# Optimization experiments

Hardware: AMD Instinct MI355X
Metric: run time of the kernel (lower is better)

## Reference

```python
import jax, jax.numpy as jnp
import numpy as np

N_X = 50000      # real nodes
N_MOTIF = 10000  # motif nodes
N = N_X + N_MOTIF
E = 1_920_000    # edges (avg degree 32)
NFEAT = 512
NHID = 256
PAD_N = 65536


def setup_inputs() -> dict:
    key = jax.random.key(0)
    ks = jax.random.split(key, 12)
    x = jax.random.normal(ks[0], (N_X, NFEAT), dtype=jnp.float32)
    motif_emb = jax.random.normal(ks[1], (N_MOTIF, NFEAT), dtype=jnp.float32)
    adj_rows = jax.random.randint(ks[2], (E,), 0, N)
    adj_cols = jax.random.randint(ks[3], (E,), 0, N)
    adj_vals = jax.random.uniform(ks[4], (E,), dtype=jnp.float32)
    # unique scatter positions (torch output[pos_idx]=x with distinct indices)
    pos_idx = jax.random.permutation(ks[5], PAD_N)[:N_X]
    # GraphConvolution params (pygcn style: support = x@W; out = spmm(adj, support) + b)
    s1 = 1.0 / np.sqrt(NHID)
    w1 = jax.random.uniform(ks[6], (NFEAT, NHID), minval=-s1, maxval=s1, dtype=jnp.float32)
    b1 = jax.random.uniform(ks[7], (NHID,), minval=-s1, maxval=s1, dtype=jnp.float32)
    w2 = jax.random.uniform(ks[8], (NHID, NHID), minval=-s1, maxval=s1, dtype=jnp.float32)
    b2 = jax.random.uniform(ks[9], (NHID,), minval=-s1, maxval=s1, dtype=jnp.float32)
    w3 = jax.random.uniform(ks[10], (NHID, NHID), minval=-s1, maxval=s1, dtype=jnp.float32)
    b3 = jax.random.uniform(ks[11], (NHID,), minval=-s1, maxval=s1, dtype=jnp.float32)
    return {"x": x, "motif_emb": motif_emb, "adj_rows": adj_rows, "adj_cols": adj_cols,
            "adj_vals": adj_vals, "pos_idx": pos_idx, "pad_n": PAD_N,
            "w1": w1, "b1": b1, "w2": w2, "b2": b2, "w3": w3, "b3": b3}


def _gcn_layer(h, rows, cols, vals, w, b):
    support = h @ w                                   # [N, nhid]
    msgs = vals[:, None] * support[cols]              # [E, nhid]
    agg = jax.ops.segment_sum(msgs, rows, num_segments=N)  # spmm(adj, support)
    return jax.nn.relu(agg + b)


def reference(x, motif_emb, adj_rows, adj_cols, adj_vals, pos_idx, pad_n,
              w1, b1, w2, b2, w3, b3):
    h = jnp.concatenate((x, motif_emb), axis=0)       # [N, nfeat]
    h = _gcn_layer(h, adj_rows, adj_cols, adj_vals, w1, b1)
    # dropout is identity in eval mode
    h = _gcn_layer(h, adj_rows, adj_cols, adj_vals, w2, b2)
    h = _gcn_layer(h, adj_rows, adj_cols, adj_vals, w3, b3)
    h = h[:N_X]                                       # drop motif nodes
    output = jnp.zeros((pad_n, h.shape[1]), dtype=h.dtype)
    output = output.at[pos_idx].set(h)                # irregular scatter-assign
    return output
```

## Files before the change

### kernel.cpp

```cpp
#include <hip/hip_runtime.h>

#define N_TOTAL 60000
#define N_X     50000
#define N_EDGE  1920000
#define NFEAT   512
#define NHID    256
#define SLOTS   96
#define NCHUNK  8

typedef __attribute__((ext_vector_type(8))) short bf16x8;
typedef __attribute__((ext_vector_type(4))) float f32x4;
typedef __attribute__((ext_vector_type(4))) unsigned u32x4;

__device__ __forceinline__ unsigned short f2bf(float f) {
    unsigned u = __float_as_uint(f);
    unsigned r = (u + 0x7FFFu + ((u >> 16) & 1u)) >> 16;
    return (unsigned short)r;
}
__device__ __forceinline__ float bf_lo(unsigned u) { return __uint_as_float(u << 16); }
__device__ __forceinline__ float bf_hi(unsigned u) { return __uint_as_float(u & 0xFFFF0000u); }

__global__ __launch_bounds__(256)
void cvt_w_all_kernel(const float* __restrict__ w1, const float* __restrict__ w2,
                      const float* __restrict__ w3, short* __restrict__ w1T,
                      short* __restrict__ w2T, short* __restrict__ w3T)
{
    int n = blockIdx.x;
    for (int k = threadIdx.x; k < NFEAT; k += 256)
        w1T[(size_t)n * NFEAT + k] = (short)f2bf(w1[(size_t)k * NHID + n]);
    for (int k = threadIdx.x; k < NHID; k += 256)
        w2T[(size_t)n * NHID + k] = (short)f2bf(w2[(size_t)k * NHID + n]);
    for (int k = threadIdx.x; k < NHID; k += 256)
        w3T[(size_t)n * NHID + k] = (short)f2bf(w3[(size_t)k * NHID + n]);
}

#define LDA 40

template<bool AF32>
__global__ __launch_bounds__(512)
void gemm_bt_kernel(const float* __restrict__ Af, const float* __restrict__ A2f, int split,
                    const short* __restrict__ Ab, const short* __restrict__ BT,
                    short* __restrict__ C, int M, int K)
{
    __shared__ short As[128 * LDA];
    __shared__ short Bs[256 * LDA];
    const int t    = threadIdx.x;
    const int lane = t & 63;
    const int wave = t >> 6;
    const int wm   = wave & 1;
    const int wn   = wave >> 1;
    const int l16  = lane & 15;
    const int quad = lane >> 4;
    const int bm   = blockIdx.x * 128;

    f32x4 acc[4][4] = {};

    const int arow = t >> 2;
    const int asch = t & 3;
    const int brow = t >> 1;
    const int bh   = t & 1;

    for (int kk = 0; kk < K; kk += 32) {
        if (AF32) {
            int row = bm + arow;
            float4 v0 = {}, v1 = {};
            if (row < M) {
                const float* src = (row < split) ? (Af + (size_t)row * K)
                                                 : (A2f + (size_t)(row - split) * K);
                const float4* p = (const float4*)(src + kk + asch * 8);
                v0 = p[0]; v1 = p[1];
            }
            short tmp[8] = {
                (short)f2bf(v0.x), (short)f2bf(v0.y), (short)f2bf(v0.z), (short)f2bf(v0.w),
                (short)f2bf(v1.x), (short)f2bf(v1.y), (short)f2bf(v1.z), (short)f2bf(v1.w)};
            *(bf16x8*)&As[arow * LDA + asch * 8] = *(const bf16x8*)tmp;
        } else {
            bf16x8 va = {};
            int row = bm + arow;
            if (row < M) va = *(const bf16x8*)(Ab + (size_t)row * K + kk + asch * 8);
            *(bf16x8*)&As[arow * LDA + asch * 8] = va;
        }
        {
            const short* src = BT + (size_t)brow * K + kk + bh * 16;
            *(bf16x8*)&Bs[brow * LDA + bh * 16]     = *(const bf16x8*)(src);
            *(bf16x8*)&Bs[brow * LDA + bh * 16 + 8] = *(const bf16x8*)(src + 8);
        }
        __syncthreads();

        bf16x8 af[4], bfr[4];
        #pragma unroll
        for (int i = 0; i < 4; i++) {
            af[i]  = *(const bf16x8*)&As[(wm * 64 + i * 16 + l16) * LDA + quad * 8];
            bfr[i] = *(const bf16x8*)&Bs[(wn * 64 + i * 16 + l16) * LDA + quad * 8];
        }
        #pragma unroll
        for (int i = 0; i < 4; i++)
            #pragma unroll
            for (int j = 0; j < 4; j++)
                acc[i][j] = __builtin_amdgcn_mfma_f32_16x16x32_bf16(af[i], bfr[j], acc[i][j], 0, 0, 0);
        __syncthreads();
    }

    #pragma unroll
    for (int i = 0; i < 4; i++) {
        #pragma unroll
        for (int r = 0; r < 4; r++) {
            int row = bm + wm * 64 + i * 16 + quad * 4 + r;
            if (row < M) {
                #pragma unroll
                for (int j = 0; j < 4; j++) {
                    int col = wn * 64 + j * 16 + l16;
                    size_t idx = (size_t)(col >> 5) * M * 32 + (size_t)row * 32 + (col & 31);
                    __builtin_nontemporal_store((short)f2bf(acc[i][j][r]), C + idx);
                }
            }
        }
    }
}

__global__ __launch_bounds__(256)
void init_cursor_kernel(int* __restrict__ cursor)
{
    int i = blockIdx.x * 256 + threadIdx.x;
    if (i < N_TOTAL) cursor[i] = i * SLOTS;
}

__global__ __launch_bounds__(256)
void scatter_edges_kernel(const int* __restrict__ rows, const int* __restrict__ cols,
                          const float* __restrict__ vals, int* __restrict__ cursor,
                          unsigned* __restrict__ edges)
{
    const int b = blockIdx.x;
    const int g = b & 7;
    const int i = (b >> 3) * 256 + threadIdx.x;
    const int lo = g * (N_TOTAL / 8);
    const int hi = lo + (N_TOTAL / 8);
    int r = __builtin_nontemporal_load(&rows[i]);
    if (r >= lo && r < hi) {
        unsigned rec = (unsigned)cols[i] | ((unsigned)f2bf(vals[i]) << 16);
        int p = atomicAdd(&cursor[r], 1);
        edges[p] = rec;
    }
}

template<int MODE>
__global__ __launch_bounds__(256)
void spmm_relu_kernel(const int* __restrict__ row_end, const unsigned* __restrict__ edges,
                      const u32x4* __restrict__ supportC, const float* __restrict__ bias,
                      u32x4* __restrict__ out_bf, float* __restrict__ out_f32,
                      const int* __restrict__ pos, int nrows)
{
    const int chunk = blockIdx.x & 7;
    const int grp   = blockIdx.x >> 3;
    const int wave  = threadIdx.x >> 6;
    const int lane  = threadIdx.x & 63;
    const int gid   = lane >> 2;
    const int fl    = lane & 3;
    const int rbase = grp * 64 + wave * 16;
    if (rbase >= nrows) return;
    const int r  = rbase + gid;
    const int rc = min(r, nrows - 1);
    const int start = rc * SLOTS;
    const int len   = row_end[rc] - start;
    const u32x4* __restrict__ sb = supportC + (size_t)chunk * N_TOTAL * 4 + fl;
    const u32x4* __restrict__ ep = (const u32x4*)(edges + start);

    float a[8] = {};
    u32x4 e0 = ep[0];
    u32x4 e1 = ep[1];
    for (int it = 0; it < len; it += 8) {
        const int g = it >> 2;
        u32x4 n0 = ep[g + 2];
        u32x4 n1 = ep[g + 3];
        #pragma unroll
        for (int s = 0; s < 4; s++) {
            unsigned es = e0[s];
            u32x4 u = sb[(size_t)(es & 0xFFFFu) * 4];
            float w = bf_hi(es);
            #pragma unroll
            for (int k = 0; k < 4; k++) {
                a[2*k]     += w * bf_lo(u[k]);
                a[2*k + 1] += w * bf_hi(u[k]);
            }
        }
        #pragma unroll
        for (int s = 0; s < 4; s++) {
            unsigned es = e1[s];
            u32x4 u = sb[(size_t)(es & 0xFFFFu) * 4];
            float w = bf_hi(es);
            #pragma unroll
            for (int k = 0; k < 4; k++) {
                a[2*k]     += w * bf_lo(u[k]);
                a[2*k + 1] += w * bf_hi(u[k]);
            }
        }
        e0 = n0; e1 = n1;
    }

    const f32x4* bb = (const f32x4*)bias + chunk * 8 + fl * 2;
    f32x4 bv0 = bb[0], bv1 = bb[1];
    float o[8];
    #pragma unroll
    for (int k = 0; k < 8; k++) {
        float bk = (k < 4) ? bv0[k] : bv1[k - 4];
        o[k] = fmaxf(a[k] + bk, 0.f);
    }
    if (r < nrows) {
        if (MODE == 1) {
            f32x4 q0 = {o[0], o[1], o[2], o[3]};
            f32x4 q1 = {o[4], o[5], o[6], o[7]};
            f32x4* dst = (f32x4*)out_f32 + (size_t)pos[r] * 64 + chunk * 8 + fl * 2;
            __builtin_nontemporal_store(q0, dst);
            __builtin_nontemporal_store(q1, dst + 1);
        } else {
            u32x4 q;
            #pragma unroll
            for (int k = 0; k < 4; k++)
                q[k] = (unsigned)f2bf(o[2*k]) | ((unsigned)f2bf(o[2*k + 1]) << 16);
            __builtin_nontemporal_store(q, out_bf + (size_t)r * 32 + chunk * 4 + fl);
        }
    }
}

extern "C" void kernel_launch(void* const* d_in, const int* in_sizes, int n_in,
                              void* d_out, int out_size, void* d_ws, size_t ws_size,
                              hipStream_t stream)
{
    const float* x     = (const float*)d_in[0];
    const float* motif = (const float*)d_in[1];
    const int*   rows  = (const int*)d_in[2];
    const int*   cols  = (const int*)d_in[3];
    const float* vals  = (const float*)d_in[4];
    const int*   pos   = (const int*)d_in[5];
    const float* w1 = (const float*)d_in[7];
    const float* b1 = (const float*)d_in[8];
    const float* w2 = (const float*)d_in[9];
    const float* b2 = (const float*)d_in[10];
    const float* w3 = (const float*)d_in[11];
    const float* b3 = (const float*)d_in[12];
    (void)ws_size; (void)n_in; (void)in_sizes;

    char* ws = (char*)d_ws;
    size_t off = 0;
    short* h_bf     = (short*)(ws + off); off += (size_t)N_TOTAL * NHID * 2;
    short* support  = (short*)(ws + off); off += (size_t)N_TOTAL * NHID * 2;
    short* w1T      = (short*)(ws + off); off += (size_t)NHID * NFEAT * 2;
    short* w2T      = (short*)(ws + off); off += (size_t)NHID * NHID * 2;
    short* w3T      = (short*)(ws + off); off += (size_t)NHID * NHID * 2;
    int* cursor     = (int*)(ws + off);   off += 60032 * 4;
    unsigned* edges = (unsigned*)(ws + off); off += (size_t)N_TOTAL * SLOTS * 4 + 256;

    hipMemsetAsync(d_out, 0, (size_t)out_size * sizeof(float), stream);
    hipMemsetAsync(edges, 0, (size_t)N_TOTAL * SLOTS * 4, stream);
    cvt_w_all_kernel<<<NHID, 256, 0, stream>>>(w1, w2, w3, w1T, w2T, w3T);
    init_cursor_kernel<<<(N_TOTAL + 255) / 256, 256, 0, stream>>>(cursor);
    scatter_edges_kernel<<<(N_EDGE / 256) * 8, 256, 0, stream>>>(rows, cols, vals, cursor, edges);

    const int ggrid = (N_TOTAL + 127) / 128;
    const int sgrid0 = ((N_TOTAL + 63) / 64) * NCHUNK;
    const int sgrid1 = ((N_X + 63) / 64) * NCHUNK;

    gemm_bt_kernel<true><<<ggrid, 512, 0, stream>>>(x, motif, N_X, nullptr, w1T, support, N_TOTAL, NFEAT);
    spmm_relu_kernel<0><<<sgrid0, 256, 0, stream>>>(cursor, edges, (const u32x4*)support, b1,
                                                    (u32x4*)h_bf, nullptr, nullptr, N_TOTAL);
    gemm_bt_kernel<false><<<ggrid, 512, 0, stream>>>(nullptr, nullptr, 0, h_bf, w2T, support, N_TOTAL, NHID);
    spmm_relu_kernel<0><<<sgrid0, 256, 0, stream>>>(cursor, edges, (const u32x4*)support, b2,
                                                    (u32x4*)h_bf, nullptr, nullptr, N_TOTAL);
    gemm_bt_kernel<false><<<ggrid, 512, 0, stream>>>(nullptr, nullptr, 0, h_bf, w3T, support, N_TOTAL, NHID);
    spmm_relu_kernel<1><<<sgrid1, 256, 0, stream>>>(cursor, edges, (const u32x4*)support, b3,
                                                    nullptr, (float*)d_out, pos, N_X);
}
```

Before: 696.3 us.

## Stage row edge lists in LDS and process all feature chunks per block

Before, each block handled one of 8 feature chunks, so every row's edge list was read from global memory once per chunk. Now each block owns 32 rows, copies their edge records (96 slots) into shared memory once, and loops over 4 chunk pairs, gathering two support slices per edge. This cuts redundant edge-list loads and the row_end lookups repeated per chunk. In exchange the block size drops to 128 threads, the grid is 8x smaller, and register pressure rises from the doubled accumulators, so parallelism and gather concurrency may fall.

```diff
diff --git a/kernel.cpp b/kernel.cpp
--- a/kernel.cpp
+++ b/kernel.cpp
@@ -7,6 +7,7 @@
 #define NHID    256
 #define SLOTS   96
 #define NCHUNK  8
+#define LSTR    100
 
 typedef __attribute__((ext_vector_type(8))) short bf16x8;
 typedef __attribute__((ext_vector_type(4))) float f32x4;
@@ -144,80 +145,108 @@
 }
 
 template<int MODE>
-__global__ __launch_bounds__(256)
+__global__ __launch_bounds__(128)
 void spmm_relu_kernel(const int* __restrict__ row_end, const unsigned* __restrict__ edges,
                       const u32x4* __restrict__ supportC, const float* __restrict__ bias,
                       u32x4* __restrict__ out_bf, float* __restrict__ out_f32,
                       const int* __restrict__ pos, int nrows)
 {
-    const int chunk = blockIdx.x & 7;
-    const int grp   = blockIdx.x >> 3;
+    __shared__ unsigned s_edge[2][16 * LSTR];
     const int wave  = threadIdx.x >> 6;
     const int lane  = threadIdx.x & 63;
     const int gid   = lane >> 2;
     const int fl    = lane & 3;
-    const int rbase = grp * 64 + wave * 16;
+    const int rbase = blockIdx.x * 32 + wave * 16;
     if (rbase >= nrows) return;
-    const int r  = rbase + gid;
-    const int rc = min(r, nrows - 1);
-    const int start = rc * SLOTS;
-    const int len   = row_end[rc] - start;
-    const u32x4* __restrict__ sb = supportC + (size_t)chunk * N_TOTAL * 4 + fl;
-    const u32x4* __restrict__ ep = (const u32x4*)(edges + start);
-
-    float a[8] = {};
-    u32x4 e0 = ep[0];
-    u32x4 e1 = ep[1];
-    for (int it = 0; it < len; it += 8) {
-        const int g = it >> 2;
-        u32x4 n0 = ep[g + 2];
-        u32x4 n1 = ep[g + 3];
-        #pragma unroll
-        for (int s = 0; s < 4; s++) {
-            unsigned es = e0[s];
-            u32x4 u = sb[(size_t)(es & 0xFFFFu) * 4];
-            float w = bf_hi(es);
+    const int r   = rbase + gid;
+    const int rc  = min(r, nrows - 1);
+    const int len = row_end[rc] - rc * SLOTS;
+
+    {
+        const u32x4* src = (const u32x4*)(edges + (size_t)rc * SLOTS);
+        u32x4* dst = (u32x4*)&s_edge[wave][gid * LSTR];
+        #pragma unroll
+        for (int j = 0; j < 6; j++)
+            dst[j * 4 + fl] = src[j * 4 + fl];
+    }
+    asm volatile("s_waitcnt lgkmcnt(0)" ::: "memory");
+    __builtin_amdgcn_sched_barrier(0);
+
+    const unsigned* eL = &s_edge[wave][gid * LSTR];
+    const size_t slice = (size_t)N_TOTAL * 4;
+
+    #pragma unroll 1
+    for (int c = 0; c < 4; c++) {
+        const u32x4* __restrict__ sb0 = supportC + (size_t)c * slice + fl;
+        const u32x4* __restrict__ sb1 = sb0 + 4 * slice;
+        float a0[8] = {}, a1[8] = {};
+        for (int it = 0; it < len; it += 8) {
+            u32x4 e0 = *(const u32x4*)&eL[it];
+            u32x4 e1 = *(const u32x4*)&eL[it + 4];
             #pragma unroll
-            for (int k = 0; k < 4; k++) {
-                a[2*k]     += w * bf_lo(u[k]);
-                a[2*k + 1] += w * bf_hi(u[k]);
-            }
-        }
-        #pragma unroll
-        for (int s = 0; s < 4; s++) {
-            unsigned es = e1[s];
-            u32x4 u = sb[(size_t)(es & 0xFFFFu) * 4];
-            float w = bf_hi(es);
+            for (int s = 0; s < 4; s++) {
+                unsigned es = e0[s];
+                size_t co = (size_t)(es & 0xFFFFu) * 4;
+                u32x4 u0 = sb0[co];
+                u32x4 u1 = sb1[co];
+                float w = bf_hi(es);
+                #pragma unroll
+                for (int k = 0; k < 4; k++) {
+                    a0[2*k]     += w * bf_lo(u0[k]);
+                    a0[2*k + 1] += w * bf_hi(u0[k]);
+                    a1[2*k]     += w * bf_lo(u1[k]);
+                    a1[2*k + 1] += w * bf_hi(u1[k]);
+                }
+            }
             #pragma unroll
-            for (int k = 0; k < 4; k++) {
-                a[2*k]     += w * bf_lo(u[k]);
-                a[2*k + 1] += w * bf_hi(u[k]);
-            }
-        }
-        e0 = n0; e1 = n1;
-    }
-
-    const f32x4* bb = (const f32x4*)bias + chunk * 8 + fl * 2;
-    f32x4 bv0 = bb[0], bv1 = bb[1];
-    float o[8];
-    #pragma unroll
-    for (int k = 0; k < 8; k++) {
-        float bk = (k < 4) ? bv0[k] : bv1[k - 4];
-        o[k] = fmaxf(a[k] + bk, 0.f);
-    }
-    if (r < nrows) {
-        if (MODE == 1) {
-            f32x4 q0 = {o[0], o[1], o[2], o[3]};
-            f32x4 q1 = {o[4], o[5], o[6], o[7]};
-            f32x4* dst = (f32x4*)out_f32 + (size_t)pos[r] * 64 + chunk * 8 + fl * 2;
-            __builtin_nontemporal_store(q0, dst);
-            __builtin_nontemporal_store(q1, dst + 1);
-        } else {
-            u32x4 q;
-            #pragma unroll
-            for (int k = 0; k < 4; k++)
-                q[k] = (unsigned)f2bf(o[2*k]) | ((unsigned)f2bf(o[2*k + 1]) << 16);
-            __builtin_nontemporal_store(q, out_bf + (size_t)r * 32 + chunk * 4 + fl);
+            for (int s = 0; s < 4; s++) {
+                unsigned es = e1[s];
+                size_t co = (size_t)(es & 0xFFFFu) * 4;
+                u32x4 u0 = sb0[co];
+                u32x4 u1 = sb1[co];
+                float w = bf_hi(es);
+                #pragma unroll
+                for (int k = 0; k < 4; k++) {
+                    a0[2*k]     += w * bf_lo(u0[k]);
+                    a0[2*k + 1] += w * bf_hi(u0[k]);
+                    a1[2*k]     += w * bf_lo(u1[k]);
+                    a1[2*k + 1] += w * bf_hi(u1[k]);
+                }
+            }
+        }
+
+        const f32x4* bbl = (const f32x4*)bias + c * 8 + fl * 2;
+        const f32x4* bbh = (const f32x4*)bias + (c + 4) * 8 + fl * 2;
+        f32x4 b0l = bbl[0], b1l = bbl[1], b0h = bbh[0], b1h = bbh[1];
+        float o0[8], o1[8];
+        #pragma unroll
+        for (int k = 0; k < 8; k++) {
+            float bkl = (k < 4) ? b0l[k] : b1l[k - 4];
+            float bkh = (k < 4) ? b0h[k] : b1h[k - 4];
+            o0[k] = fmaxf(a0[k] + bkl, 0.f);
+            o1[k] = fmaxf(a1[k] + bkh, 0.f);
+        }
+        if (r < nrows) {
+            if (MODE == 1) {
+                f32x4* dst = (f32x4*)out_f32 + (size_t)pos[r] * 64;
+                f32x4 q0 = {o0[0], o0[1], o0[2], o0[3]};
+                f32x4 q1 = {o0[4], o0[5], o0[6], o0[7]};
+                f32x4 q2 = {o1[0], o1[1], o1[2], o1[3]};
+                f32x4 q3 = {o1[4], o1[5], o1[6], o1[7]};
+                __builtin_nontemporal_store(q0, dst + c * 8 + fl * 2);
+                __builtin_nontemporal_store(q1, dst + c * 8 + fl * 2 + 1);
+                __builtin_nontemporal_store(q2, dst + (c + 4) * 8 + fl * 2);
+                __builtin_nontemporal_store(q3, dst + (c + 4) * 8 + fl * 2 + 1);
+            } else {
+                u32x4 q0, q1;
+                #pragma unroll
+                for (int k = 0; k < 4; k++) {
+                    q0[k] = (unsigned)f2bf(o0[2*k]) | ((unsigned)f2bf(o0[2*k + 1]) << 16);
+                    q1[k] = (unsigned)f2bf(o1[2*k]) | ((unsigned)f2bf(o1[2*k + 1]) << 16);
+                }
+                __builtin_nontemporal_store(q0, out_bf + (size_t)r * 32 + c * 4 + fl);
+                __builtin_nontemporal_store(q1, out_bf + (size_t)r * 32 + (c + 4) * 4 + fl);
+            }
         }
     }
 }
@@ -257,16 +286,16 @@
     scatter_edges_kernel<<<(N_EDGE / 256) * 8, 256, 0, stream>>>(rows, cols, vals, cursor, edges);
 
     const int ggrid = (N_TOTAL + 127) / 128;
-    const int sgrid0 = ((N_TOTAL + 63) / 64) * NCHUNK;
-    const int sgrid1 = ((N_X + 63) / 64) * NCHUNK;
+    const int sgrid0 = (N_TOTAL + 31) / 32;
+    const int sgrid1 = (N_X + 31) / 32;
 
     gemm_bt_kernel<true><<<ggrid, 512, 0, stream>>>(x, motif, N_X, nullptr, w1T, support, N_TOTAL, NFEAT);
-    spmm_relu_kernel<0><<<sgrid0, 256, 0, stream>>>(cursor, edges, (const u32x4*)support, b1,
+    spmm_relu_kernel<0><<<sgrid0, 128, 0, stream>>>(cursor, edges, (const u32x4*)support, b1,
                                                     (u32x4*)h_bf, nullptr, nullptr, N_TOTAL);
     gemm_bt_kernel<false><<<ggrid, 512, 0, stream>>>(nullptr, nullptr, 0, h_bf, w2T, support, N_TOTAL, NHID);
-    spmm_relu_kernel<0><<<sgrid0, 256, 0, stream>>>(cursor, edges, (const u32x4*)support, b2,
+    spmm_relu_kernel<0><<<sgrid0, 128, 0, stream>>>(cursor, edges, (const u32x4*)support, b2,
                                                     (u32x4*)h_bf, nullptr, nullptr, N_TOTAL);
     gemm_bt_kernel<false><<<ggrid, 512, 0, stream>>>(nullptr, nullptr, 0, h_bf, w3T, support, N_TOTAL, NHID);
-    spmm_relu_kernel<1><<<sgrid1, 256, 0, stream>>>(cursor, edges, (const u32x4*)support, b3,
+    spmm_relu_kernel<1><<<sgrid1, 128, 0, stream>>>(cursor, edges, (const u32x4*)support, b3,
                                                     nullptr, (float*)d_out, pos, N_X);
 }
```

Result: slower. 940.9 us (+35.1%).
